# Optimization experiments

Measured on AMD Instinct MI355X. Metric: run time of the kernel, lower is better.

Reference implementation:

```python
import math
import jax, jax.numpy as jnp
import numpy as np

NUM_SLICES = 1024
NUM_TEST_POINTS = 17
INV_WEIGHT = 25.0
SIGREG_WEIGHT = 25.0
EPS = 1e-6


def _reference_points():
    # erfinv(2*q - 1) * sqrt(2) for q = linspace(0.01, 0.99, K)
    q = jnp.linspace(0.01, 0.99, NUM_TEST_POINTS)
    return jax.scipy.special.erfinv(2.0 * q - 1.0) * math.sqrt(2.0)


def _sigreg_loss(z, a, g):
    # z: [N, D], a: [M, D] unit slice directions, g: [K] reference points
    proj = z @ a.T                      # [N, M]
    x = proj.T                          # [M, N]
    mu = x.mean(axis=1, keepdims=True)
    sd = jnp.std(x, axis=1, ddof=1, keepdims=True) + EPS  # torch.std is unbiased
    xs = (x - mu) / sd                  # [M, N] standardized projections
    N = xs.shape[1]
    K = g.shape[0]
    # term1: (1/N^2) sum_ij exp(-0.5 (x_i - x_j)^2)   -> pairwise [M, N, N]
    t1 = jnp.exp(-0.5 * (xs[:, :, None] - xs[:, None, :]) ** 2).sum(axis=(1, 2)) / (N * N)
    # term2: -(2/(N K)) sum_ik exp(-0.5 (x_i - g_k)^2) -> [M, N, K]
    t2 = -2.0 * jnp.exp(-0.5 * (xs[:, :, None] - g[None, None, :]) ** 2).sum(axis=(1, 2)) / (N * K)
    # term3: (1/K^2) sum_kl exp(-0.5 (g_k - g_l)^2)    -> scalar
    t3 = jnp.exp(-0.5 * (g[:, None] - g[None, :]) ** 2).sum() / (K * K)
    return (t1 + t2 + t3).mean()


def setup_inputs() -> dict:
    key = jax.random.key(0)
    k1, k2, k3 = jax.random.split(key, 3)
    z_a = jax.random.normal(k1, (256, 768), dtype=jnp.float32)
    z_b = jax.random.normal(k2, (256, 768), dtype=jnp.float32)
    slices = jax.random.normal(k3, (NUM_SLICES, 768), dtype=jnp.float32)
    return {"z_a": z_a, "z_b": z_b, "slices": slices}


def reference(z_a, z_b, slices):
    # invariance (MSE) term
    inv_loss = jnp.mean((z_a - z_b) ** 2)
    # normalize slice directions to the unit sphere (F.normalize, eps=1e-12)
    norm = jnp.maximum(jnp.linalg.norm(slices, axis=1, keepdims=True), 1e-12)
    a = slices / norm
    g = _reference_points()
    sigreg_a = _sigreg_loss(z_a, a, g)
    sigreg_b = _sigreg_loss(z_b, a, g)
    sigreg = 0.5 * (sigreg_a + sigreg_b)
    total = INV_WEIGHT * inv_loss + SIGREG_WEIGHT * sigreg
    return total
```

## Files before the change

kernel.cpp:

```cpp
#include <hip/hip_runtime.h>
#include <hip/hip_bf16.h>
#include <math.h>

#define NSLICES 1024
#define DIM     768
#define NPTS    256
#define K_REF   17
#define KSPLIT  8
#define KCHUNK  (DIM / KSPLIT)
#define XSZ     (NSLICES * NPTS)

#define INV_OFF 0
#define G_OFF   208
#define SIG_OFF 256
#define XP_OFF  2560

#define EXP2(x) __builtin_amdgcn_exp2f(x)
#define SCALE_A 0.84932180028801904272f
#define INV_N2  1.52587890625e-05f
#define T2_SC   4.595588235294118e-4f

__device__ __forceinline__ float wave_sum(float v) {
#pragma unroll
    for (int o = 32; o; o >>= 1) v += __shfl_xor(v, o, 64);
    return v;
}

__device__ __forceinline__ float block_sum_256(float v, float* wred, int tid) {
    v = wave_sum(v);
    if ((tid & 63) == 0) wred[tid >> 6] = v;
    __syncthreads();
    float r = wred[0] + wred[1] + wred[2] + wred[3];
    __syncthreads();
    return r;
}

__global__ __launch_bounds__(256) void inv_kernel(const float* __restrict__ za,
                                                  const float* __restrict__ zb,
                                                  float* __restrict__ w) {
    __shared__ float wred[4];
    int tid = threadIdx.x;
    int idx = blockIdx.x * 256 + tid;
    const float4* A = (const float4*)za;
    const float4* B = (const float4*)zb;
    float4 a = A[idx], b = B[idx];
    float dx = a.x - b.x, dy = a.y - b.y, dz = a.z - b.z, dw = a.w - b.w;
    float p = dx * dx + dy * dy + dz * dz + dw * dw;
    float s = block_sum_256(p, wred, tid);
    if (tid == 0) w[INV_OFF + blockIdx.x] = s;
    if (blockIdx.x == 0 && tid < K_REF) {
        float q = 0.01f + 0.06125f * (float)tid;
        w[G_OFF + tid] = erfinvf(2.0f * q - 1.0f) * 1.41421356237309504880f * SCALE_A;
    }
}

__global__ __launch_bounds__(256) void proj_kernel(const float* __restrict__ za,
                                                   const float* __restrict__ zb,
                                                   const float* __restrict__ slices,
                                                   float* __restrict__ w, int npart) {
    __shared__ float sA[16][68];
    __shared__ float sB[16][68];
    const int nt = blockIdx.x;
    const int mt = blockIdx.y;
    const int zi = blockIdx.z >> 3;
    const int kc = blockIdx.z & 7;
    const float* Z = zi ? zb : za;
    const int m0 = mt * 64, n0 = nt * 64;
    const int tid = threadIdx.x;
    const int tx = tid & 15, ty = tid >> 4;
    const int lr = tid >> 2, lq = tid & 3;
    const int kbase = kc * KCHUNK;

    float acc[4][4] = {};

    for (int k0 = 0; k0 < KCHUNK; k0 += 16) {
        float4 av = *(const float4*)(slices + (size_t)(m0 + lr) * DIM + kbase + k0 + lq * 4);
        float4 bv = *(const float4*)(Z + (size_t)(n0 + lr) * DIM + kbase + k0 + lq * 4);
        sA[lq * 4 + 0][lr] = av.x; sA[lq * 4 + 1][lr] = av.y;
        sA[lq * 4 + 2][lr] = av.z; sA[lq * 4 + 3][lr] = av.w;
        sB[lq * 4 + 0][lr] = bv.x; sB[lq * 4 + 1][lr] = bv.y;
        sB[lq * 4 + 2][lr] = bv.z; sB[lq * 4 + 3][lr] = bv.w;
        __syncthreads();
#pragma unroll
        for (int kk = 0; kk < 16; ++kk) {
            float4 a = *(const float4*)&sA[kk][ty * 4];
            float4 b = *(const float4*)&sB[kk][tx * 4];
            acc[0][0] += a.x * b.x; acc[0][1] += a.x * b.y; acc[0][2] += a.x * b.z; acc[0][3] += a.x * b.w;
            acc[1][0] += a.y * b.x; acc[1][1] += a.y * b.y; acc[1][2] += a.y * b.z; acc[1][3] += a.y * b.w;
            acc[2][0] += a.z * b.x; acc[2][1] += a.z * b.y; acc[2][2] += a.z * b.z; acc[2][3] += a.z * b.w;
            acc[3][0] += a.w * b.x; acc[3][1] += a.w * b.y; acc[3][2] += a.w * b.z; acc[3][3] += a.w * b.w;
        }
        __syncthreads();
    }

    if (npart == KSPLIT) {
        float* X = w + XP_OFF + ((size_t)zi * KSPLIT + kc) * XSZ;
#pragma unroll
        for (int i = 0; i < 4; ++i) {
            float4 o; o.x = acc[i][0]; o.y = acc[i][1]; o.z = acc[i][2]; o.w = acc[i][3];
            *(float4*)(X + (size_t)(m0 + ty * 4 + i) * NPTS + n0 + tx * 4) = o;
        }
    } else {
        float* X = w + XP_OFF + (size_t)zi * XSZ;
#pragma unroll
        for (int i = 0; i < 4; ++i)
#pragma unroll
            for (int j = 0; j < 4; ++j)
                atomicAdd(X + (size_t)(m0 + ty * 4 + i) * NPTS + n0 + tx * 4 + j, acc[i][j]);
    }
}

template <int NPART>
__global__ __launch_bounds__(256) void sigreg_kernel(float* __restrict__ w) {
    __shared__ __align__(16) float ys[2 * NPTS];
    __shared__ float gsh[K_REF];
    __shared__ float wredA[4], wredB[4];
    const int m = blockIdx.x;
    const int zi = blockIdx.y;
    const int tid = threadIdx.x;

    const float* Xb = w + XP_OFF + (size_t)zi * NPART * XSZ + (size_t)m * NPTS + tid;
    float xp[NPART];
#pragma unroll
    for (int p = 0; p < NPART; ++p) xp[p] = Xb[(size_t)p * XSZ];
    if (tid < K_REF) gsh[tid] = w[G_OFF + tid];
    float xv = 0.f;
#pragma unroll
    for (int p = 0; p < NPART; ++p) xv += xp[p];

    float r1 = wave_sum(xv);
    float r2 = wave_sum(xv * xv);
    if ((tid & 63) == 0) { wredA[tid >> 6] = r1; wredB[tid >> 6] = r2; }
    __syncthreads();
    float sumx  = (wredA[0] + wredA[1]) + (wredA[2] + wredA[3]);
    float sumx2 = (wredB[0] + wredB[1]) + (wredB[2] + wredB[3]);
    float mu = sumx * (1.0f / NPTS);
    float ss = sumx2 - mu * sumx;
    float sd = sqrtf(ss * (1.0f / (NPTS - 1))) + 1e-6f;
    float yv = (xv - mu) / sd * SCALE_A;
    ys[tid] = yv;
    ys[tid + NPTS] = yv;
    __syncthreads();

    float a0 = 0.f, a1 = 0.f, a2 = 0.f, a3 = 0.f;
#pragma unroll
    for (int t = 0; t < 32; ++t) {
        float d0 = yv - ys[tid + 4 * t + 1];
        float d1 = yv - ys[tid + 4 * t + 2];
        float d2 = yv - ys[tid + 4 * t + 3];
        float d3 = yv - ys[tid + 4 * t + 4];
        a0 += EXP2(-(d0 * d0));
        a1 += EXP2(-(d1 * d1));
        a2 += EXP2(-(d2 * d2));
        a3 += EXP2(-(d3 * d3));
    }
    float dl = yv - ys[tid + 128];
    float s128 = EXP2(-(dl * dl));
    float sg = 0.f;
#pragma unroll
    for (int k = 0; k < K_REF; ++k) {
        float d = yv - gsh[k];
        sg += EXP2(-(d * d));
    }
    float c = (2.0f * ((a0 + a1) + (a2 + a3)) - s128) * INV_N2 - sg * T2_SC;
    if (tid == 0) c += (float)NPTS * INV_N2;
    float v = wave_sum(c);
    if ((tid & 63) == 0) wredA[tid >> 6] = v;
    __syncthreads();
    if (tid == 0) {
        float tot = (wredA[0] + wredA[1]) + (wredA[2] + wredA[3]);
        w[SIG_OFF + zi * NSLICES + m] = tot * (0.5f / (float)NSLICES);
    }
}

__global__ __launch_bounds__(256) void final_kernel(const float* __restrict__ w,
                                                    float* __restrict__ out) {
    __shared__ float wred[4];
    __shared__ float gsh[K_REF];
    const int tid = threadIdx.x;
    if (tid < K_REF) gsh[tid] = w[G_OFF + tid];
    float sv = 0.f;
    for (int i = tid; i < 2 * NSLICES; i += 256) sv += w[SIG_OFF + i];
    float iv = (tid < 192) ? w[INV_OFF + tid] : 0.f;
    float sig = block_sum_256(sv, wred, tid);
    float inv = block_sum_256(iv, wred, tid);
    float t3p = 0.f;
    for (int idx = tid; idx < K_REF * K_REF; idx += 256) {
        int k = idx / K_REF, l = idx - k * K_REF;
        float d = gsh[k] - gsh[l];
        t3p += EXP2(-(d * d));
    }
    float t3 = block_sum_256(t3p, wred, tid) * (1.0f / ((float)K_REF * (float)K_REF));
    if (tid == 0) {
        out[0] = 25.0f * inv * (1.0f / ((float)NPTS * (float)DIM))
               + 25.0f * (sig + t3);
    }
}

extern "C" void kernel_launch(void* const* d_in, const int* in_sizes, int n_in,
                              void* d_out, int out_size, void* d_ws, size_t ws_size,
                              hipStream_t stream) {
    const float* za = (const float*)d_in[0];
    const float* zb = (const float*)d_in[1];
    const float* slices = (const float*)d_in[2];
    float* out = (float*)d_out;
    float* w = (float*)d_ws;

    const size_t need_full = (size_t)(XP_OFF + 2 * KSPLIT * XSZ) * sizeof(float);
    const int npart = (ws_size >= need_full) ? KSPLIT : 1;

    if (npart == 1)
        hipMemsetAsync(w + XP_OFF, 0, (size_t)2 * XSZ * sizeof(float), stream);

    inv_kernel<<<192, 256, 0, stream>>>(za, zb, w);
    dim3 pg(4, 16, 2 * KSPLIT);
    proj_kernel<<<pg, 256, 0, stream>>>(za, zb, slices, w, npart);
    dim3 sg(NSLICES, 2);
    if (npart == KSPLIT)
        sigreg_kernel<KSPLIT><<<sg, 256, 0, stream>>>(w);
    else
        sigreg_kernel<1><<<sg, 256, 0, stream>>>(w);
    final_kernel<<<1, 256, 0, stream>>>(w, out);
}
```

Baseline: 97.91 us.

## Use bf16 MFMA for projection GEMM with split-K reduced to 4

Replaces the FP32 scalar-FMA tiled GEMM in the projection kernel with bf16 MFMA 16x16x32 instructions. Each block converts its whole 64x192 K-chunk of slices and embeddings to bf16 in shared memory once and then issues MFMAs per wave. Split-K drops from 8 to 4, which halves the partial-sum planes that the sigreg kernel must read. The cost is lower projection precision from bf16 rounding, which may disturb the standardized values and the Gaussian-kernel loss, plus fewer blocks in the GEMM grid.

New measurement: 86.99 us. -11.1%, faster.

```diff
diff --git a/kernel.cpp b/kernel.cpp
--- a/kernel.cpp
+++ b/kernel.cpp
@@ -6,9 +6,10 @@
 #define DIM     768
 #define NPTS    256
 #define K_REF   17
-#define KSPLIT  8
+#define KSPLIT  4
 #define KCHUNK  (DIM / KSPLIT)
 #define XSZ     (NSLICES * NPTS)
+#define LPITCH  200
 
 #define INV_OFF 0
 #define G_OFF   208
@@ -20,6 +21,9 @@
 #define INV_N2  1.52587890625e-05f
 #define T2_SC   4.595588235294118e-4f
 
+typedef __attribute__((ext_vector_type(8))) short bf16x8_t;
+typedef __attribute__((ext_vector_type(4))) float f32x4_t;
+
 __device__ __forceinline__ float wave_sum(float v) {
 #pragma unroll
     for (int o = 32; o; o >>= 1) v += __shfl_xor(v, o, 64);
@@ -33,6 +37,11 @@
     float r = wred[0] + wred[1] + wred[2] + wred[3];
     __syncthreads();
     return r;
+}
+
+__device__ __forceinline__ unsigned f2bf(float f) {
+    unsigned u = __float_as_uint(f);
+    return (u + 0x7FFFu + ((u >> 16) & 1u)) >> 16;
 }
 
 __global__ __launch_bounds__(256) void inv_kernel(const float* __restrict__ za,
@@ -58,55 +67,80 @@
                                                    const float* __restrict__ zb,
                                                    const float* __restrict__ slices,
                                                    float* __restrict__ w, int npart) {
-    __shared__ float sA[16][68];
-    __shared__ float sB[16][68];
+    __shared__ unsigned short lA[64][LPITCH];
+    __shared__ unsigned short lB[64][LPITCH];
     const int nt = blockIdx.x;
     const int mt = blockIdx.y;
-    const int zi = blockIdx.z >> 3;
-    const int kc = blockIdx.z & 7;
+    const int zi = blockIdx.z >> 2;
+    const int kc = blockIdx.z & 3;
     const float* Z = zi ? zb : za;
     const int m0 = mt * 64, n0 = nt * 64;
     const int tid = threadIdx.x;
-    const int tx = tid & 15, ty = tid >> 4;
-    const int lr = tid >> 2, lq = tid & 3;
     const int kbase = kc * KCHUNK;
 
-    float acc[4][4] = {};
-
-    for (int k0 = 0; k0 < KCHUNK; k0 += 16) {
-        float4 av = *(const float4*)(slices + (size_t)(m0 + lr) * DIM + kbase + k0 + lq * 4);
-        float4 bv = *(const float4*)(Z + (size_t)(n0 + lr) * DIM + kbase + k0 + lq * 4);
-        sA[lq * 4 + 0][lr] = av.x; sA[lq * 4 + 1][lr] = av.y;
-        sA[lq * 4 + 2][lr] = av.z; sA[lq * 4 + 3][lr] = av.w;
-        sB[lq * 4 + 0][lr] = bv.x; sB[lq * 4 + 1][lr] = bv.y;
-        sB[lq * 4 + 2][lr] = bv.z; sB[lq * 4 + 3][lr] = bv.w;
-        __syncthreads();
-#pragma unroll
-        for (int kk = 0; kk < 16; ++kk) {
-            float4 a = *(const float4*)&sA[kk][ty * 4];
-            float4 b = *(const float4*)&sB[kk][tx * 4];
-            acc[0][0] += a.x * b.x; acc[0][1] += a.x * b.y; acc[0][2] += a.x * b.z; acc[0][3] += a.x * b.w;
-            acc[1][0] += a.y * b.x; acc[1][1] += a.y * b.y; acc[1][2] += a.y * b.z; acc[1][3] += a.y * b.w;
-            acc[2][0] += a.z * b.x; acc[2][1] += a.z * b.y; acc[2][2] += a.z * b.z; acc[2][3] += a.z * b.w;
-            acc[3][0] += a.w * b.x; acc[3][1] += a.w * b.y; acc[3][2] += a.w * b.z; acc[3][3] += a.w * b.w;
+    {
+        const int r = tid >> 2;
+        const int c4 = tid & 3;
+        const float* Ap = slices + (size_t)(m0 + r) * DIM + kbase + c4 * 4;
+        const float* Bp = Z + (size_t)(n0 + r) * DIM + kbase + c4 * 4;
+        unsigned short* la = &lA[r][c4 * 4];
+        unsigned short* lb = &lB[r][c4 * 4];
+#pragma unroll
+        for (int i = 0; i < 12; ++i) {
+            float4 av = *(const float4*)(Ap + i * 16);
+            float4 bv = *(const float4*)(Bp + i * 16);
+            uint2 ap, bp;
+            ap.x = f2bf(av.x) | (f2bf(av.y) << 16);
+            ap.y = f2bf(av.z) | (f2bf(av.w) << 16);
+            bp.x = f2bf(bv.x) | (f2bf(bv.y) << 16);
+            bp.y = f2bf(bv.z) | (f2bf(bv.w) << 16);
+            *(uint2*)(la + i * 16) = ap;
+            *(uint2*)(lb + i * 16) = bp;
         }
-        __syncthreads();
-    }
-
+    }
+    __syncthreads();
+
+    const int wv = tid >> 6;
+    const int wr = wv >> 1, wc = wv & 1;
+    const int lane = tid & 63;
+    const int fr = lane & 15, fq = lane >> 4;
+
+    f32x4_t acc00 = {0.f, 0.f, 0.f, 0.f}, acc01 = acc00, acc10 = acc00, acc11 = acc00;
+    const int ra0 = wr * 32 + fr, ra1 = ra0 + 16;
+    const int rb0 = wc * 32 + fr, rb1 = rb0 + 16;
+#pragma unroll
+    for (int ks = 0; ks < KCHUNK / 32; ++ks) {
+        const int k0 = ks * 32 + fq * 8;
+        bf16x8_t a0 = *(const bf16x8_t*)&lA[ra0][k0];
+        bf16x8_t a1 = *(const bf16x8_t*)&lA[ra1][k0];
+        bf16x8_t b0 = *(const bf16x8_t*)&lB[rb0][k0];
+        bf16x8_t b1 = *(const bf16x8_t*)&lB[rb1][k0];
+        acc00 = __builtin_amdgcn_mfma_f32_16x16x32_bf16(a0, b0, acc00, 0, 0, 0);
+        acc01 = __builtin_amdgcn_mfma_f32_16x16x32_bf16(a0, b1, acc01, 0, 0, 0);
+        acc10 = __builtin_amdgcn_mfma_f32_16x16x32_bf16(a1, b0, acc10, 0, 0, 0);
+        acc11 = __builtin_amdgcn_mfma_f32_16x16x32_bf16(a1, b1, acc11, 0, 0, 0);
+    }
+
+    const int rowB = m0 + wr * 32 + fq * 4;
+    const int colB = n0 + wc * 32 + fr;
     if (npart == KSPLIT) {
         float* X = w + XP_OFF + ((size_t)zi * KSPLIT + kc) * XSZ;
 #pragma unroll
-        for (int i = 0; i < 4; ++i) {
-            float4 o; o.x = acc[i][0]; o.y = acc[i][1]; o.z = acc[i][2]; o.w = acc[i][3];
-            *(float4*)(X + (size_t)(m0 + ty * 4 + i) * NPTS + n0 + tx * 4) = o;
+        for (int j = 0; j < 4; ++j) {
+            X[(size_t)(rowB + j) * NPTS + colB]           = acc00[j];
+            X[(size_t)(rowB + j) * NPTS + colB + 16]      = acc01[j];
+            X[(size_t)(rowB + 16 + j) * NPTS + colB]      = acc10[j];
+            X[(size_t)(rowB + 16 + j) * NPTS + colB + 16] = acc11[j];
         }
     } else {
         float* X = w + XP_OFF + (size_t)zi * XSZ;
 #pragma unroll
-        for (int i = 0; i < 4; ++i)
-#pragma unroll
-            for (int j = 0; j < 4; ++j)
-                atomicAdd(X + (size_t)(m0 + ty * 4 + i) * NPTS + n0 + tx * 4 + j, acc[i][j]);
+        for (int j = 0; j < 4; ++j) {
+            atomicAdd(X + (size_t)(rowB + j) * NPTS + colB,           acc00[j]);
+            atomicAdd(X + (size_t)(rowB + j) * NPTS + colB + 16,      acc01[j]);
+            atomicAdd(X + (size_t)(rowB + 16 + j) * NPTS + colB,      acc10[j]);
+            atomicAdd(X + (size_t)(rowB + 16 + j) * NPTS + colB + 16, acc11[j]);
+        }
     }
 }
 
```
